# Performance work log

Measured on AMD Instinct MI355X. Metric: run time of the kernel, lower is better.

The kernel has to match this reference:

```python
import jax, jax.numpy as jnp
import numpy as np

B, C, S, H, Wd = 512, 32, 8, 6, 6   # batch, in_channels, size_primary_caps, in_h, in_w
O, OW = 10, 16                      # out_height, out_width
IN_CAPS = C * H * Wd                # 1152
ITER = 3                            # routing iterations


def setup_inputs() -> dict:
    key = jax.random.key(0)
    k1, k2 = jax.random.split(key)
    x = jax.random.normal(k1, (B, C, S, H, Wd), dtype=jnp.float32)
    stdv = 1.0 / np.sqrt(S)
    W = jax.random.uniform(k2, (1, O, IN_CAPS, OW, S), dtype=jnp.float32,
                           minval=-stdv, maxval=stdv)
    return {"x": x, "W": W}


def squash(s, axis=-1):
    n2 = jnp.sum(s * s, axis=axis, keepdims=True)
    return (n2 / (1.0 + n2)) * s / jnp.sqrt(n2)


def reference(x, W):
    bsz = x.shape[0]
    # torch: x.reshape(b,1,-1,S,1); row-major reshape is identical in jnp
    xr = x.reshape(bsz, IN_CAPS, S)             # [B, in_caps, S]
    # W @ x : [1,O,I,OW,S] @ [B,1,I,S,1] -> [B,O,I,OW]
    u = jnp.einsum('oiws,bis->boiw', W[0], xr)  # [B, O, in_caps, OW]
    b = jnp.zeros((bsz, O, IN_CAPS, 1), dtype=u.dtype)
    v = None
    for _ in range(ITER):
        c = jax.nn.softmax(b, axis=1)           # softmax over out_height (dim=-3)
        s = jnp.sum(u * c, axis=2)              # [B, O, OW]
        v = squash(s, axis=-1)                  # [B, O, OW]
        agreement = jnp.einsum('boiw,bow->boi', u, v)[..., None]
        b = b + agreement
    return v
```

## Files before the change

kernel.cpp:

```cpp
#include <hip/hip_runtime.h>
#include <cstddef>
#include <cstdint>


typedef _Float16 h2 __attribute__((ext_vector_type(2)));
typedef __fp16 fp16v2 __attribute__((ext_vector_type(2)));

constexpr int O_ = 10, I_ = 1152, W_ = 16, S_ = 8;
constexpr int BQ = 2;
constexpr int NTH = 1024, NWV = 16;
constexpr int SLOTS = NWV * 4;
constexpr int KSEQ = I_ / SLOTS;
constexpr int WROW = O_ * W_ * S_;

union U32H2 { uint32_t u; h2 h; fp16v2 f; };
__device__ __forceinline__ h2 as_h2(uint32_t u) { U32H2 c; c.u = u; return c.h; }
__device__ __forceinline__ uint32_t as_u32(h2 h) { U32H2 c; c.h = h; return c.u; }
__device__ __forceinline__ h2 cvt_pk(float a, float b) {
  U32H2 c; c.f = __builtin_amdgcn_cvt_pkrtz(a, b); return c.h;
}

constexpr int W4TOT = O_ * I_ * W_ * S_ / 4;
__global__ __launch_bounds__(256) void wprep(const float4* __restrict__ Wg,
                                             uint2* __restrict__ Wt) {
  int idx = blockIdx.x * 256 + threadIdx.x;
  if (idx >= W4TOT) return;
  int w2 = idx & 31;
  int oi = idx >> 5;
  int o = oi / I_;
  int i = oi - o * I_;
  float4 v = Wg[idx];
  uint2 pk;
  pk.x = as_u32(cvt_pk(v.x, v.y));
  pk.y = as_u32(cvt_pk(v.z, v.w));
  Wt[(i * O_ + o) * 32 + w2] = pk;
}

__device__ __forceinline__ float dot8(const uint4& wv, const uint32_t* xr) {
  return __builtin_amdgcn_fdot2(as_h2(wv.x), as_h2(xr[0]),
          __builtin_amdgcn_fdot2(as_h2(wv.y), as_h2(xr[1]),
           __builtin_amdgcn_fdot2(as_h2(wv.z), as_h2(xr[2]),
            __builtin_amdgcn_fdot2(as_h2(wv.w), as_h2(xr[3]),
                                   0.f, false), false), false), false);
}

__global__ __launch_bounds__(NTH, 1) void digitcaps_fused(
    const float* __restrict__ xg, const _Float16* __restrict__ Wt,
    float* __restrict__ out) {
  __shared__ _Float16 xl[BQ * I_ * S_];
  __shared__ float s_buf[NWV][BQ][O_][W_];
  __shared__ float vcur[BQ][O_ * W_];
  __shared__ float v1s[BQ][O_ * W_];

  const int tid = threadIdx.x, blk = blockIdx.x;
  const int wave = tid >> 6, lane = tid & 63;
  const int wg = lane & 15;
  const int isub = lane >> 4;

  {
    const float4* xb = (const float4*)(xg + (size_t)blk * (BQ * I_ * S_));
    uint2* xw = (uint2*)xl;
#pragma unroll
    for (int j = 0; j < 5; ++j) {
      int f = j * NTH + tid;
      if (f < BQ * I_ * S_ / 4) {
        float4 v = xb[f];
        uint2 pk;
        pk.x = as_u32(cvt_pk(v.x, v.y));
        pk.y = as_u32(cvt_pk(v.z, v.w));
        xw[f] = pk;
      }
    }
  }
  __syncthreads();

  const int ib = wave * 4 + isub;

  {
    float S[BQ][O_];
#pragma unroll
    for (int b = 0; b < BQ; ++b)
#pragma unroll
      for (int o = 0; o < O_; ++o) S[b][o] = 0.f;

#pragma unroll 2
    for (int k = 0; k < KSEQ; ++k) {
      const int i = ib + SLOTS * k;
      uint32_t xr[BQ][4];
#pragma unroll
      for (int b = 0; b < BQ; ++b) {
        uint4 t = *(const uint4*)&xl[(b * I_ + i) * S_];
        xr[b][0] = t.x; xr[b][1] = t.y; xr[b][2] = t.z; xr[b][3] = t.w;
      }
      const _Float16* wi = Wt + (size_t)i * WROW + wg * S_;
#pragma unroll
      for (int o = 0; o < O_; ++o) {
        uint4 wv = *(const uint4*)(wi + o * (W_ * S_));
#pragma unroll
        for (int b = 0; b < BQ; ++b) S[b][o] += dot8(wv, xr[b]);
      }
    }
#pragma unroll
    for (int b = 0; b < BQ; ++b)
#pragma unroll
      for (int o = 0; o < O_; ++o) {
        float s = S[b][o];
        s += __shfl_xor(s, 16);
        s += __shfl_xor(s, 32);
        S[b][o] = s;
      }
    if (isub == 0) {
#pragma unroll
      for (int b = 0; b < BQ; ++b)
#pragma unroll
        for (int o = 0; o < O_; ++o) s_buf[wave][b][o][wg] = S[b][o];
    }
    __syncthreads();

    if (tid < BQ * O_ * W_) {
      const int bb = tid / (O_ * W_);
      const int r = tid % (O_ * W_);
      float s = 0.f;
#pragma unroll
      for (int wv = 0; wv < NWV; ++wv) s += s_buf[wv][bb][r >> 4][r & 15];
      s *= 0.1f;
      float n2 = s * s;
      n2 += __shfl_xor(n2, 1);
      n2 += __shfl_xor(n2, 2);
      n2 += __shfl_xor(n2, 4);
      n2 += __shfl_xor(n2, 8);
      const float v = s * sqrtf(n2) / (1.0f + n2);
      vcur[bb][r] = v;
      v1s[bb][r] = v;
    }
    __syncthreads();
  }

  for (int pass = 1; pass < 3; ++pass) {
    h2 vrpk[O_];
#pragma unroll
    for (int o = 0; o < O_; ++o)
      vrpk[o] = cvt_pk(vcur[0][o * W_ + wg], vcur[1][o * W_ + wg]);
    h2 Spk[O_];
#pragma unroll
    for (int o = 0; o < O_; ++o) Spk[o] = h2{(_Float16)0, (_Float16)0};

#pragma unroll 2
    for (int k = 0; k < KSEQ; ++k) {
      const int i = ib + SLOTS * k;
      uint32_t xr[BQ][4];
#pragma unroll
      for (int b = 0; b < BQ; ++b) {
        uint4 t = *(const uint4*)&xl[(b * I_ + i) * S_];
        xr[b][0] = t.x; xr[b][1] = t.y; xr[b][2] = t.z; xr[b][3] = t.w;
      }
      const _Float16* wi = Wt + (size_t)i * WROW + wg * S_;
      h2 upk[O_], ppk[O_];
#pragma unroll
      for (int o = 0; o < O_; ++o) {
        uint4 wv = *(const uint4*)(wi + o * (W_ * S_));
        float u0 = dot8(wv, xr[0]);
        float u1 = dot8(wv, xr[1]);
        upk[o] = cvt_pk(u0, u1);
        ppk[o] = upk[o] * vrpk[o];
      }
#pragma unroll
      for (int o = 0; o < O_; ++o) {
#pragma unroll
        for (int d = 1; d <= 8; d <<= 1)
          ppk[o] = ppk[o] + as_h2((uint32_t)__shfl_xor((int)as_u32(ppk[o]), d));
      }
      float e0[O_], e1[O_];
      float es0 = 0.f, es1 = 0.f;
#pragma unroll
      for (int o = 0; o < O_; ++o) {
        e0[o] = __expf((float)ppk[o][0]); es0 += e0[o];
        e1[o] = __expf((float)ppk[o][1]); es1 += e1[o];
      }
      const float inv0 = 1.0f / es0, inv1 = 1.0f / es1;
#pragma unroll
      for (int o = 0; o < O_; ++o) {
        h2 c = cvt_pk(e0[o] * inv0, e1[o] * inv1);
        Spk[o] = Spk[o] + c * upk[o];
      }
    }

#pragma unroll
    for (int o = 0; o < O_; ++o) {
      Spk[o] = Spk[o] + as_h2((uint32_t)__shfl_xor((int)as_u32(Spk[o]), 16));
      Spk[o] = Spk[o] + as_h2((uint32_t)__shfl_xor((int)as_u32(Spk[o]), 32));
    }
    if (isub == 0) {
#pragma unroll
      for (int o = 0; o < O_; ++o) {
        s_buf[wave][0][o][wg] = (float)Spk[o][0];
        s_buf[wave][1][o][wg] = (float)Spk[o][1];
      }
    }
    __syncthreads();

    if (tid < BQ * O_ * W_) {
      const int bb = tid / (O_ * W_);
      const int r = tid % (O_ * W_);
      float s = 0.f;
#pragma unroll
      for (int wv = 0; wv < NWV; ++wv) s += s_buf[wv][bb][r >> 4][r & 15];
      float n2 = s * s;
      n2 += __shfl_xor(n2, 1);
      n2 += __shfl_xor(n2, 2);
      n2 += __shfl_xor(n2, 4);
      n2 += __shfl_xor(n2, 8);
      const float v = s * sqrtf(n2) / (1.0f + n2);
      if (pass == 1)  vcur[bb][r] = v1s[bb][r] + v;
      else            out[((size_t)(blk * BQ) + bb) * (O_ * W_) + r] = v;
    }
    __syncthreads();
  }
}

extern "C" void kernel_launch(void* const* d_in, const int* in_sizes, int n_in,
                              void* d_out, int out_size, void* d_ws, size_t ws_size,
                              hipStream_t stream) {
  const float* x = (const float*)d_in[0];
  const float* W = (const float*)d_in[1];
  float* out = (float*)d_out;
  _Float16* Wt = (_Float16*)d_ws;

  hipLaunchKernelGGL(wprep, dim3((W4TOT + 255) / 256), dim3(256), 0, stream,
                     (const float4*)W, (uint2*)Wt);
  hipLaunchKernelGGL(digitcaps_fused, dim3(512 / BQ), dim3(NTH), 0, stream,
                     x, Wt, out);
}
```

Before: 156.6 us.

## Cache prediction vectors in registers and process one batch per block

The kernel now computes the u predictions once in the first pass and keeps them packed in registers (u[5][18] half2) for the two routing passes. Before, each pass recomputed them from W read out of global memory. The packing changes from batch pairs to output-capsule pairs, so each block handles a single batch element and the grid doubles to 512 blocks. This removes two extra sweeps over W and the dot products behind them. In exchange, W reuse across two batch elements is lost, global W traffic per batch element doubles in the first pass, and register pressure rises.

```diff
diff --git a/kernel.cpp b/kernel.cpp
--- a/kernel.cpp
+++ b/kernel.cpp
@@ -7,10 +7,10 @@
 typedef __fp16 fp16v2 __attribute__((ext_vector_type(2)));
 
 constexpr int O_ = 10, I_ = 1152, W_ = 16, S_ = 8;
-constexpr int BQ = 2;
 constexpr int NTH = 1024, NWV = 16;
 constexpr int SLOTS = NWV * 4;
 constexpr int KSEQ = I_ / SLOTS;
+constexpr int OQ = O_ / 2;
 constexpr int WROW = O_ * W_ * S_;
 
 union U32H2 { uint32_t u; h2 h; fp16v2 f; };
@@ -47,23 +47,24 @@
 __global__ __launch_bounds__(NTH, 1) void digitcaps_fused(
     const float* __restrict__ xg, const _Float16* __restrict__ Wt,
     float* __restrict__ out) {
-  __shared__ _Float16 xl[BQ * I_ * S_];
-  __shared__ float s_buf[NWV][BQ][O_][W_];
-  __shared__ float vcur[BQ][O_ * W_];
-  __shared__ float v1s[BQ][O_ * W_];
+  __shared__ _Float16 xl[I_ * S_];
+  __shared__ float s_buf[NWV][O_][W_];
+  __shared__ float vcur[O_ * W_];
+  __shared__ float v1s[O_ * W_];
 
   const int tid = threadIdx.x, blk = blockIdx.x;
   const int wave = tid >> 6, lane = tid & 63;
   const int wg = lane & 15;
   const int isub = lane >> 4;
+  const int ib = wave * 4 + isub;
 
   {
-    const float4* xb = (const float4*)(xg + (size_t)blk * (BQ * I_ * S_));
+    const float4* xb = (const float4*)(xg + (size_t)blk * (I_ * S_));
     uint2* xw = (uint2*)xl;
 #pragma unroll
-    for (int j = 0; j < 5; ++j) {
+    for (int j = 0; j < 3; ++j) {
       int f = j * NTH + tid;
-      if (f < BQ * I_ * S_ / 4) {
+      if (f < I_ * S_ / 4) {
         float4 v = xb[f];
         uint2 pk;
         pk.x = as_u32(cvt_pk(v.x, v.y));
@@ -74,55 +75,51 @@
   }
   __syncthreads();
 
-  const int ib = wave * 4 + isub;
+  h2 u[OQ][KSEQ];
 
   {
-    float S[BQ][O_];
-#pragma unroll
-    for (int b = 0; b < BQ; ++b)
-#pragma unroll
-      for (int o = 0; o < O_; ++o) S[b][o] = 0.f;
-
-#pragma unroll 2
+    float S0[O_];
+#pragma unroll
+    for (int o = 0; o < O_; ++o) S0[o] = 0.f;
+
+#pragma unroll
     for (int k = 0; k < KSEQ; ++k) {
       const int i = ib + SLOTS * k;
-      uint32_t xr[BQ][4];
-#pragma unroll
-      for (int b = 0; b < BQ; ++b) {
-        uint4 t = *(const uint4*)&xl[(b * I_ + i) * S_];
-        xr[b][0] = t.x; xr[b][1] = t.y; xr[b][2] = t.z; xr[b][3] = t.w;
+      uint32_t xr[4];
+      {
+        uint4 t = *(const uint4*)&xl[i * S_];
+        xr[0] = t.x; xr[1] = t.y; xr[2] = t.z; xr[3] = t.w;
       }
       const _Float16* wi = Wt + (size_t)i * WROW + wg * S_;
 #pragma unroll
-      for (int o = 0; o < O_; ++o) {
-        uint4 wv = *(const uint4*)(wi + o * (W_ * S_));
-#pragma unroll
-        for (int b = 0; b < BQ; ++b) S[b][o] += dot8(wv, xr[b]);
-      }
-    }
-#pragma unroll
-    for (int b = 0; b < BQ; ++b)
-#pragma unroll
-      for (int o = 0; o < O_; ++o) {
-        float s = S[b][o];
-        s += __shfl_xor(s, 16);
-        s += __shfl_xor(s, 32);
-        S[b][o] = s;
-      }
+      for (int oq = 0; oq < OQ; ++oq) {
+        uint4 wv0 = *(const uint4*)(wi + (2 * oq) * (W_ * S_));
+        uint4 wv1 = *(const uint4*)(wi + (2 * oq + 1) * (W_ * S_));
+        float f0 = dot8(wv0, xr);
+        float f1 = dot8(wv1, xr);
+        u[oq][k] = cvt_pk(f0, f1);
+        S0[2 * oq] += f0;
+        S0[2 * oq + 1] += f1;
+      }
+    }
+#pragma unroll
+    for (int o = 0; o < O_; ++o) {
+      float s = S0[o];
+      s += __shfl_xor(s, 16);
+      s += __shfl_xor(s, 32);
+      S0[o] = s;
+    }
     if (isub == 0) {
 #pragma unroll
-      for (int b = 0; b < BQ; ++b)
-#pragma unroll
-        for (int o = 0; o < O_; ++o) s_buf[wave][b][o][wg] = S[b][o];
-    }
-    __syncthreads();
-
-    if (tid < BQ * O_ * W_) {
-      const int bb = tid / (O_ * W_);
-      const int r = tid % (O_ * W_);
+      for (int o = 0; o < O_; ++o) s_buf[wave][o][wg] = S0[o];
+    }
+    __syncthreads();
+
+    if (tid < O_ * W_) {
+      const int r = tid;
       float s = 0.f;
 #pragma unroll
-      for (int wv = 0; wv < NWV; ++wv) s += s_buf[wv][bb][r >> 4][r & 15];
+      for (int wv = 0; wv < NWV; ++wv) s += s_buf[wv][r >> 4][r & 15];
       s *= 0.1f;
       float n2 = s * s;
       n2 += __shfl_xor(n2, 1);
@@ -130,89 +127,75 @@
       n2 += __shfl_xor(n2, 4);
       n2 += __shfl_xor(n2, 8);
       const float v = s * sqrtf(n2) / (1.0f + n2);
-      vcur[bb][r] = v;
-      v1s[bb][r] = v;
+      vcur[r] = v;
+      v1s[r] = v;
     }
     __syncthreads();
   }
 
   for (int pass = 1; pass < 3; ++pass) {
-    h2 vrpk[O_];
-#pragma unroll
-    for (int o = 0; o < O_; ++o)
-      vrpk[o] = cvt_pk(vcur[0][o * W_ + wg], vcur[1][o * W_ + wg]);
-    h2 Spk[O_];
-#pragma unroll
-    for (int o = 0; o < O_; ++o) Spk[o] = h2{(_Float16)0, (_Float16)0};
-
-#pragma unroll 2
+    h2 vrpk[OQ];
+#pragma unroll
+    for (int oq = 0; oq < OQ; ++oq)
+      vrpk[oq] = cvt_pk(vcur[(2 * oq) * W_ + wg], vcur[(2 * oq + 1) * W_ + wg]);
+
+    float S[O_];
+#pragma unroll
+    for (int o = 0; o < O_; ++o) S[o] = 0.f;
+
+#pragma unroll
     for (int k = 0; k < KSEQ; ++k) {
-      const int i = ib + SLOTS * k;
-      uint32_t xr[BQ][4];
-#pragma unroll
-      for (int b = 0; b < BQ; ++b) {
-        uint4 t = *(const uint4*)&xl[(b * I_ + i) * S_];
-        xr[b][0] = t.x; xr[b][1] = t.y; xr[b][2] = t.z; xr[b][3] = t.w;
-      }
-      const _Float16* wi = Wt + (size_t)i * WROW + wg * S_;
-      h2 upk[O_], ppk[O_];
-#pragma unroll
-      for (int o = 0; o < O_; ++o) {
-        uint4 wv = *(const uint4*)(wi + o * (W_ * S_));
-        float u0 = dot8(wv, xr[0]);
-        float u1 = dot8(wv, xr[1]);
-        upk[o] = cvt_pk(u0, u1);
-        ppk[o] = upk[o] * vrpk[o];
-      }
-#pragma unroll
-      for (int o = 0; o < O_; ++o) {
+      h2 ppk[OQ];
+#pragma unroll
+      for (int oq = 0; oq < OQ; ++oq) ppk[oq] = u[oq][k] * vrpk[oq];
+#pragma unroll
+      for (int oq = 0; oq < OQ; ++oq) {
 #pragma unroll
         for (int d = 1; d <= 8; d <<= 1)
-          ppk[o] = ppk[o] + as_h2((uint32_t)__shfl_xor((int)as_u32(ppk[o]), d));
-      }
-      float e0[O_], e1[O_];
-      float es0 = 0.f, es1 = 0.f;
-#pragma unroll
-      for (int o = 0; o < O_; ++o) {
-        e0[o] = __expf((float)ppk[o][0]); es0 += e0[o];
-        e1[o] = __expf((float)ppk[o][1]); es1 += e1[o];
-      }
-      const float inv0 = 1.0f / es0, inv1 = 1.0f / es1;
-#pragma unroll
-      for (int o = 0; o < O_; ++o) {
-        h2 c = cvt_pk(e0[o] * inv0, e1[o] * inv1);
-        Spk[o] = Spk[o] + c * upk[o];
+          ppk[oq] = ppk[oq] + as_h2((uint32_t)__shfl_xor((int)as_u32(ppk[oq]), d));
+      }
+      float e[O_];
+      float es = 0.f;
+#pragma unroll
+      for (int oq = 0; oq < OQ; ++oq) {
+        e[2 * oq]     = __expf((float)ppk[oq][0]);
+        e[2 * oq + 1] = __expf((float)ppk[oq][1]);
+        es += e[2 * oq] + e[2 * oq + 1];
+      }
+      const float inv = 1.0f / es;
+#pragma unroll
+      for (int oq = 0; oq < OQ; ++oq) {
+        S[2 * oq]     += (e[2 * oq] * inv)     * (float)u[oq][k][0];
+        S[2 * oq + 1] += (e[2 * oq + 1] * inv) * (float)u[oq][k][1];
       }
     }
 
 #pragma unroll
     for (int o = 0; o < O_; ++o) {
-      Spk[o] = Spk[o] + as_h2((uint32_t)__shfl_xor((int)as_u32(Spk[o]), 16));
-      Spk[o] = Spk[o] + as_h2((uint32_t)__shfl_xor((int)as_u32(Spk[o]), 32));
+      float s = S[o];
+      s += __shfl_xor(s, 16);
+      s += __shfl_xor(s, 32);
+      S[o] = s;
     }
     if (isub == 0) {
 #pragma unroll
-      for (int o = 0; o < O_; ++o) {
-        s_buf[wave][0][o][wg] = (float)Spk[o][0];
-        s_buf[wave][1][o][wg] = (float)Spk[o][1];
-      }
-    }
-    __syncthreads();
-
-    if (tid < BQ * O_ * W_) {
-      const int bb = tid / (O_ * W_);
-      const int r = tid % (O_ * W_);
+      for (int o = 0; o < O_; ++o) s_buf[wave][o][wg] = S[o];
+    }
+    __syncthreads();
+
+    if (tid < O_ * W_) {
+      const int r = tid;
       float s = 0.f;
 #pragma unroll
-      for (int wv = 0; wv < NWV; ++wv) s += s_buf[wv][bb][r >> 4][r & 15];
+      for (int wv = 0; wv < NWV; ++wv) s += s_buf[wv][r >> 4][r & 15];
       float n2 = s * s;
       n2 += __shfl_xor(n2, 1);
       n2 += __shfl_xor(n2, 2);
       n2 += __shfl_xor(n2, 4);
       n2 += __shfl_xor(n2, 8);
       const float v = s * sqrtf(n2) / (1.0f + n2);
-      if (pass == 1)  vcur[bb][r] = v1s[bb][r] + v;
-      else            out[((size_t)(blk * BQ) + bb) * (O_ * W_) + r] = v;
+      if (pass == 1)  vcur[r] = v1s[r] + v;
+      else            out[(size_t)blk * (O_ * W_) + r] = v;
     }
     __syncthreads();
   }
@@ -228,6 +211,6 @@
 
   hipLaunchKernelGGL(wprep, dim3((W4TOT + 255) / 256), dim3(256), 0, stream,
                      (const float4*)W, (uint2*)Wt);
-  hipLaunchKernelGGL(digitcaps_fused, dim3(512 / BQ), dim3(NTH), 0, stream,
+  hipLaunchKernelGGL(digitcaps_fused, dim3(512), dim3(NTH), 0, stream,
                      x, Wt, out);
 }
```

Result: slower. 250.5 us (+60.0%).

## Split routing passes into separate kernels with input-capsule halves per block

Applied to the files above, without the earlier changes.

Replaces the single fused kernel with three sweep kernels, one per routing pass, plus small combine kernels. Each sweep block handles half of the input capsules for a batch pair, doubling the number of blocks. Partial sums go through global memory, and a combine kernel does the squash and the v update. This trades extra launches, global round trips and repeated x loads for more blocks and possibly two blocks per CU.

```diff
diff --git a/kernel.cpp b/kernel.cpp
--- a/kernel.cpp
+++ b/kernel.cpp
@@ -9,9 +9,12 @@
 constexpr int O_ = 10, I_ = 1152, W_ = 16, S_ = 8;
 constexpr int BQ = 2;
 constexpr int NTH = 1024, NWV = 16;
+constexpr int IH = I_ / 2;
 constexpr int SLOTS = NWV * 4;
-constexpr int KSEQ = I_ / SLOTS;
+constexpr int KSEQ = IH / SLOTS;
 constexpr int WROW = O_ * W_ * S_;
+constexpr int NBP = 256;
+constexpr int OW = O_ * W_;
 
 union U32H2 { uint32_t u; h2 h; fp16v2 f; };
 __device__ __forceinline__ h2 as_h2(uint32_t u) { U32H2 c; c.u = u; return c.h; }
@@ -44,27 +47,30 @@
                                    0.f, false), false), false), false);
 }
 
-__global__ __launch_bounds__(NTH, 1) void digitcaps_fused(
+template <int PASS>
+__global__ __launch_bounds__(NTH, 8) void sweep(
     const float* __restrict__ xg, const _Float16* __restrict__ Wt,
-    float* __restrict__ out) {
-  __shared__ _Float16 xl[BQ * I_ * S_];
+    const float* __restrict__ Vcur, float* __restrict__ P) {
+  __shared__ _Float16 xl[BQ * IH * S_];
   __shared__ float s_buf[NWV][BQ][O_][W_];
-  __shared__ float vcur[BQ][O_ * W_];
-  __shared__ float v1s[BQ][O_ * W_];
 
   const int tid = threadIdx.x, blk = blockIdx.x;
+  const int bp = blk >> 1, h = blk & 1, b0 = bp * BQ;
   const int wave = tid >> 6, lane = tid & 63;
   const int wg = lane & 15;
   const int isub = lane >> 4;
+  const int ib = wave * 4 + isub;
 
   {
-    const float4* xb = (const float4*)(xg + (size_t)blk * (BQ * I_ * S_));
+    const float4* xb = (const float4*)xg;
     uint2* xw = (uint2*)xl;
 #pragma unroll
-    for (int j = 0; j < 5; ++j) {
+    for (int j = 0; j < 3; ++j) {
       int f = j * NTH + tid;
-      if (f < BQ * I_ * S_ / 4) {
-        float4 v = xb[f];
+      if (f < BQ * IH * S_ / 4) {
+        int b = f / (IH * S_ / 4);
+        int rem = f - b * (IH * S_ / 4);
+        float4 v = xb[(size_t)(b0 + b) * (I_ * S_ / 4) + h * (IH * S_ / 4) + rem];
         uint2 pk;
         pk.x = as_u32(cvt_pk(v.x, v.y));
         pk.y = as_u32(cvt_pk(v.z, v.w));
@@ -74,9 +80,7 @@
   }
   __syncthreads();
 
-  const int ib = wave * 4 + isub;
-
-  {
+  if (PASS == 0) {
     float S[BQ][O_];
 #pragma unroll
     for (int b = 0; b < BQ; ++b)
@@ -85,14 +89,15 @@
 
 #pragma unroll 2
     for (int k = 0; k < KSEQ; ++k) {
-      const int i = ib + SLOTS * k;
+      const int il = ib + SLOTS * k;
+      const int gi = h * IH + il;
       uint32_t xr[BQ][4];
 #pragma unroll
       for (int b = 0; b < BQ; ++b) {
-        uint4 t = *(const uint4*)&xl[(b * I_ + i) * S_];
+        uint4 t = *(const uint4*)&xl[(b * IH + il) * S_];
         xr[b][0] = t.x; xr[b][1] = t.y; xr[b][2] = t.z; xr[b][3] = t.w;
       }
-      const _Float16* wi = Wt + (size_t)i * WROW + wg * S_;
+      const _Float16* wi = Wt + (size_t)gi * WROW + wg * S_;
 #pragma unroll
       for (int o = 0; o < O_; ++o) {
         uint4 wv = *(const uint4*)(wi + o * (W_ * S_));
@@ -115,46 +120,27 @@
 #pragma unroll
         for (int o = 0; o < O_; ++o) s_buf[wave][b][o][wg] = S[b][o];
     }
-    __syncthreads();
-
-    if (tid < BQ * O_ * W_) {
-      const int bb = tid / (O_ * W_);
-      const int r = tid % (O_ * W_);
-      float s = 0.f;
-#pragma unroll
-      for (int wv = 0; wv < NWV; ++wv) s += s_buf[wv][bb][r >> 4][r & 15];
-      s *= 0.1f;
-      float n2 = s * s;
-      n2 += __shfl_xor(n2, 1);
-      n2 += __shfl_xor(n2, 2);
-      n2 += __shfl_xor(n2, 4);
-      n2 += __shfl_xor(n2, 8);
-      const float v = s * sqrtf(n2) / (1.0f + n2);
-      vcur[bb][r] = v;
-      v1s[bb][r] = v;
-    }
-    __syncthreads();
-  }
-
-  for (int pass = 1; pass < 3; ++pass) {
+  } else {
     h2 vrpk[O_];
 #pragma unroll
     for (int o = 0; o < O_; ++o)
-      vrpk[o] = cvt_pk(vcur[0][o * W_ + wg], vcur[1][o * W_ + wg]);
+      vrpk[o] = cvt_pk(Vcur[(size_t)(b0 + 0) * OW + o * W_ + wg],
+                       Vcur[(size_t)(b0 + 1) * OW + o * W_ + wg]);
     h2 Spk[O_];
 #pragma unroll
     for (int o = 0; o < O_; ++o) Spk[o] = h2{(_Float16)0, (_Float16)0};
 
 #pragma unroll 2
     for (int k = 0; k < KSEQ; ++k) {
-      const int i = ib + SLOTS * k;
+      const int il = ib + SLOTS * k;
+      const int gi = h * IH + il;
       uint32_t xr[BQ][4];
 #pragma unroll
       for (int b = 0; b < BQ; ++b) {
-        uint4 t = *(const uint4*)&xl[(b * I_ + i) * S_];
+        uint4 t = *(const uint4*)&xl[(b * IH + il) * S_];
         xr[b][0] = t.x; xr[b][1] = t.y; xr[b][2] = t.z; xr[b][3] = t.w;
       }
-      const _Float16* wi = Wt + (size_t)i * WROW + wg * S_;
+      const _Float16* wi = Wt + (size_t)gi * WROW + wg * S_;
       h2 upk[O_], ppk[O_];
 #pragma unroll
       for (int o = 0; o < O_; ++o) {
@@ -184,7 +170,6 @@
         Spk[o] = Spk[o] + c * upk[o];
       }
     }
-
 #pragma unroll
     for (int o = 0; o < O_; ++o) {
       Spk[o] = Spk[o] + as_h2((uint32_t)__shfl_xor((int)as_u32(Spk[o]), 16));
@@ -197,25 +182,38 @@
         s_buf[wave][1][o][wg] = (float)Spk[o][1];
       }
     }
-    __syncthreads();
-
-    if (tid < BQ * O_ * W_) {
-      const int bb = tid / (O_ * W_);
-      const int r = tid % (O_ * W_);
-      float s = 0.f;
-#pragma unroll
-      for (int wv = 0; wv < NWV; ++wv) s += s_buf[wv][bb][r >> 4][r & 15];
-      float n2 = s * s;
-      n2 += __shfl_xor(n2, 1);
-      n2 += __shfl_xor(n2, 2);
-      n2 += __shfl_xor(n2, 4);
-      n2 += __shfl_xor(n2, 8);
-      const float v = s * sqrtf(n2) / (1.0f + n2);
-      if (pass == 1)  vcur[bb][r] = v1s[bb][r] + v;
-      else            out[((size_t)(blk * BQ) + bb) * (O_ * W_) + r] = v;
-    }
-    __syncthreads();
   }
+  __syncthreads();
+
+  if (tid < BQ * OW) {
+    const int bb = tid / OW;
+    const int r = tid % OW;
+    float s = 0.f;
+#pragma unroll
+    for (int wv = 0; wv < NWV; ++wv) s += s_buf[wv][bb][r >> 4][r & 15];
+    P[((size_t)(bp * 2 + h) * BQ + bb) * OW + r] = s;
+  }
+}
+
+template <int PASS>
+__global__ __launch_bounds__(320) void combine(
+    const float* __restrict__ P, float* __restrict__ Vcur,
+    float* __restrict__ V1, float* __restrict__ out) {
+  const int bp = blockIdx.x, tid = threadIdx.x;
+  const int bb = tid / OW, r = tid % OW;
+  float s = P[((size_t)(bp * 2 + 0) * BQ + bb) * OW + r]
+          + P[((size_t)(bp * 2 + 1) * BQ + bb) * OW + r];
+  if (PASS == 0) s *= 0.1f;
+  float n2 = s * s;
+  n2 += __shfl_xor(n2, 1);
+  n2 += __shfl_xor(n2, 2);
+  n2 += __shfl_xor(n2, 4);
+  n2 += __shfl_xor(n2, 8);
+  const float v = s * sqrtf(n2) / (1.0f + n2);
+  const size_t gi = (size_t)(bp * BQ + bb) * OW + r;
+  if (PASS == 0)      { Vcur[gi] = v; V1[gi] = v; }
+  else if (PASS == 1) { Vcur[gi] = V1[gi] + v; }
+  else                { out[gi] = v; }
 }
 
 extern "C" void kernel_launch(void* const* d_in, const int* in_sizes, int n_in,
@@ -224,10 +222,18 @@
   const float* x = (const float*)d_in[0];
   const float* W = (const float*)d_in[1];
   float* out = (float*)d_out;
+
   _Float16* Wt = (_Float16*)d_ws;
+  float* P  = (float*)((char*)d_ws + 2949120);
+  float* Vc = (float*)((char*)d_ws + 2949120 + 655360);
+  float* V1 = (float*)((char*)d_ws + 2949120 + 655360 + 327680);
 
   hipLaunchKernelGGL(wprep, dim3((W4TOT + 255) / 256), dim3(256), 0, stream,
                      (const float4*)W, (uint2*)Wt);
-  hipLaunchKernelGGL(digitcaps_fused, dim3(512 / BQ), dim3(NTH), 0, stream,
-                     x, Wt, out);
-}
+  sweep<0><<<dim3(2 * NBP), dim3(NTH), 0, stream>>>(x, Wt, Vc, P);
+  combine<0><<<dim3(NBP), dim3(320), 0, stream>>>(P, Vc, V1, out);
+  sweep<1><<<dim3(2 * NBP), dim3(NTH), 0, stream>>>(x, Wt, Vc, P);
+  combine<1><<<dim3(NBP), dim3(320), 0, stream>>>(P, Vc, V1, out);
+  sweep<2><<<dim3(2 * NBP), dim3(NTH), 0, stream>>>(x, Wt, Vc, P);
+  combine<2><<<dim3(NBP), dim3(320), 0, stream>>>(P, Vc, V1, out);
+}
```

Result: slower. 183.9 us (+17.4%).
